# Kernel optimization log

Measured on AMD Instinct MI355X. Metric: run time of the kernel, lower is better.

Reference implementation:

```python
import jax, jax.numpy as jnp
import numpy as np

N_NODES = 50000
N_EDGES = 600000
N_GRAPHS = 1000
IN_DIM, HID, OUT_DIM = 100, 128, 128


def _gcn_layer(x, src, dst, W, b, n_nodes):
    # PyG GCNConv: linear -> symmetric-normalized aggregation with self-loops -> +bias
    h = x @ W                                            # [N, H]
    ones = jnp.ones((src.shape[0],), dtype=h.dtype)
    deg = jax.ops.segment_sum(ones, dst, num_segments=n_nodes) + 1.0  # +1 for self-loop
    dinv = jax.lax.rsqrt(deg)                            # deg >= 1
    norm = dinv[src] * dinv[dst]                         # [E]
    msgs = h[src] * norm[:, None]                        # [E, H] gather + scale
    agg = jax.ops.segment_sum(msgs, dst, num_segments=n_nodes)
    agg = agg + h * (dinv * dinv)[:, None]               # self-loop contribution
    return agg + b


def setup_inputs() -> dict:
    key = jax.random.key(0)
    ks = jax.random.split(key, 9)
    x = jax.random.normal(ks[0], (N_NODES, IN_DIM), dtype=jnp.float32)
    edge_index = jax.random.randint(ks[1], (2, N_EDGES), 0, N_NODES, dtype=jnp.int32)
    batch = jnp.sort(jax.random.randint(ks[2], (N_NODES,), 0, N_GRAPHS, dtype=jnp.int32))
    s = 1.0 / np.sqrt(IN_DIM)
    W1 = jax.random.uniform(ks[3], (IN_DIM, HID), minval=-s, maxval=s, dtype=jnp.float32)
    b1 = jnp.zeros((HID,), dtype=jnp.float32)
    s2 = 1.0 / np.sqrt(HID)
    W2 = jax.random.uniform(ks[4], (HID, HID), minval=-s2, maxval=s2, dtype=jnp.float32)
    b2 = jnp.zeros((HID,), dtype=jnp.float32)
    Wp = jax.random.uniform(ks[5], (HID, OUT_DIM), minval=-s2, maxval=s2, dtype=jnp.float32)
    bp = jax.random.uniform(ks[6], (OUT_DIM,), minval=-s2, maxval=s2, dtype=jnp.float32)
    return {"x": x, "edge_index": edge_index, "batch": batch,
            "W1": W1, "b1": b1, "W2": W2, "b2": b2, "Wp": Wp, "bp": bp}


def reference(x, edge_index, batch, W1, b1, W2, b2, Wp, bp):
    src, dst = edge_index[0], edge_index[1]
    h = jax.nn.relu(_gcn_layer(x, src, dst, W1, b1, N_NODES))   # dropout inactive (eval)
    h = jax.nn.relu(_gcn_layer(h, src, dst, W2, b2, N_NODES))
    # global mean pool over batch segments
    sums = jax.ops.segment_sum(h, batch, num_segments=N_GRAPHS)            # [B, H]
    cnts = jax.ops.segment_sum(jnp.ones_like(batch, dtype=h.dtype), batch,
                               num_segments=N_GRAPHS)
    pooled = sums / jnp.maximum(cnts, 1.0)[:, None]
    return pooled @ Wp + bp                                                # [B, OUT]
```

## Files before the change

kernel.cpp:

```cpp
#include <hip/hip_runtime.h>
#include <hip/hip_bf16.h>

#define N_NODES 50000
#define N_EDGES 600000
#define N_GRAPHS 1000
#define IN_DIM 100
#define HID 128
#define OUT_DIM 128
#define KP 128
#define NDSTRIDE 50048
#define NRANGE 13
#define RSHIFT 12

typedef __attribute__((ext_vector_type(8))) short bf16x8;
typedef __attribute__((ext_vector_type(4))) float f32x4;

__device__ inline unsigned short f2bf(float f) {
    __hip_bfloat16 b = __float2bfloat16(f);
    return *reinterpret_cast<unsigned short*>(&b);
}
__device__ inline float bf2f(unsigned short u) { return __uint_as_float(((unsigned int)u) << 16); }
__device__ inline float bflo(unsigned int u) { return __uint_as_float(u << 16); }
__device__ inline float bfhi(unsigned int u) { return __uint_as_float(u & 0xffff0000u); }

__global__ __launch_bounds__(256) void prep(
    const int* __restrict__ batch,
    const float* __restrict__ W1, const float* __restrict__ W2,
    unsigned short* __restrict__ wt1, unsigned short* __restrict__ wt2,
    int* __restrict__ deg_r, int* __restrict__ total, int* __restrict__ starts,
    float* __restrict__ sums)
{
    const int tid = blockIdx.x * 256 + threadIdx.x;
    const int nth = gridDim.x * 256;

    int4* z = reinterpret_cast<int4*>(deg_r);
    const int nz = (NRANGE * NDSTRIDE) / 4;
    for (int i = tid; i < nz; i += nth) z[i] = make_int4(0, 0, 0, 0);
    int4* zs = reinterpret_cast<int4*>(sums);
    for (int i = tid; i < (N_GRAPHS * HID) / 4; i += nth) zs[i] = make_int4(0, 0, 0, 0);
    if (tid == 0) total[0] = 0;

    for (int idx = tid; idx < 2 * 128 * KP; idx += nth) {
        const float* W = W1; int K = IN_DIM;
        unsigned short* wt = wt1;
        int li = idx;
        if (idx >= 128 * KP) { W = W2; K = HID; wt = wt2; li = idx - 128 * KP; }
        int n = li >> 7;
        int k = li & (KP - 1);
        float v = (k < K) ? W[(size_t)k * 128 + n] : 0.0f;
        unsigned short hi = f2bf(v);
        unsigned short lo = f2bf(v - bf2f(hi));
        size_t o = ((size_t)n << 8) + (size_t)((k >> 3) << 4) + (k & 7);
        wt[o] = hi;
        wt[o + 8] = lo;
    }

    for (int i = tid; i < N_NODES; i += nth) {
        int b = batch[i];
        if (i == 0) {
            for (int g = 0; g <= b; ++g) starts[g] = 0;
        } else {
            int pb = batch[i - 1];
            for (int g = pb + 1; g <= b; ++g) starts[g] = i;
        }
        if (i == N_NODES - 1) {
            for (int g = b + 1; g <= N_GRAPHS; ++g) starts[g] = N_NODES;
        }
    }
}

__global__ __launch_bounds__(256) void deg_count_r(
    const int* __restrict__ src, const int* __restrict__ dst, int* __restrict__ deg_r)
{
    int e = blockIdx.x * 256 + threadIdx.x;
    if (e >= N_EDGES) return;
    int d = dst[e];
    int r = src[e] >> RSHIFT;
    atomicAdd(&deg_r[r * NDSTRIDE + d], 1);
}

__global__ __launch_bounds__(256) void alloc_off_r(
    const int* __restrict__ deg_r, int* __restrict__ off, int* __restrict__ deg,
    int* __restrict__ total, float* __restrict__ dinv, int* __restrict__ cursor_r)
{
    int i = blockIdx.x * 256 + threadIdx.x;
    int pre[NRANGE];
    int v = 0;
    if (i < N_NODES) {
#pragma unroll
        for (int r = 0; r < NRANGE; r++) { pre[r] = v; v += deg_r[r * NDSTRIDE + i]; }
    }
    int lane = threadIdx.x & 63;
    int wid  = threadIdx.x >> 6;
    int x = v;
#pragma unroll
    for (int d = 1; d < 64; d <<= 1) {
        int y = __shfl_up(x, d, 64);
        if (lane >= d) x += y;
    }
    __shared__ int wsum[4];
    __shared__ int wbase[4];
    if (lane == 63) wsum[wid] = x;
    __syncthreads();
    if (threadIdx.x == 0) {
        int s0 = wsum[0], s1 = wsum[1], s2 = wsum[2], s3 = wsum[3];
        int base = atomicAdd(total, s0 + s1 + s2 + s3);
        wbase[0] = base;
        wbase[1] = base + s0;
        wbase[2] = base + s0 + s1;
        wbase[3] = base + s0 + s1 + s2;
    }
    __syncthreads();
    if (i < N_NODES) {
        int base = wbase[wid] + x - v;
        off[i] = base;
        deg[i] = v;
        dinv[i] = rsqrtf((float)v + 1.0f);
#pragma unroll
        for (int r = 0; r < NRANGE; r++) cursor_r[r * NDSTRIDE + i] = base + pre[r];
    }
}

__global__ __launch_bounds__(256) void fill_csr_r(
    const int* __restrict__ src, const int* __restrict__ dst,
    int* __restrict__ cursor_r, int* __restrict__ csr)
{
    int e = blockIdx.x * 256 + threadIdx.x;
    if (e >= N_EDGES) return;
    int d = dst[e];
    int s = src[e];
    int r = s >> RSHIFT;
    int pos = atomicAdd(&cursor_r[r * NDSTRIDE + d], 1);
    csr[pos] = s;
}

__global__ __launch_bounds__(256) void gemm_mfma(
    const float* __restrict__ A, int K, int M,
    const unsigned short* __restrict__ wt,
    const float* __restrict__ dinv, unsigned int* __restrict__ hb)
{
    const int w    = threadIdx.x >> 6;
    const int lane = threadIdx.x & 63;
    const int row_in = lane & 15;
    const int kgrp   = lane >> 4;
    const int wrow = w & 1;
    const int wcol = w >> 1;
    const int m = blockIdx.x * 32 + wrow * 16 + row_in;

    f32x4 acc[4];
#pragma unroll
    for (int j = 0; j < 4; j++) acc[j] = (f32x4){0.f, 0.f, 0.f, 0.f};

    for (int k0 = 0; k0 < K; k0 += 32) {
        int kb = k0 + kgrp * 8;
        float av[8];
#pragma unroll
        for (int i = 0; i < 8; i++) av[i] = 0.f;
        if (m < M) {
            if (kb + 8 <= K) {
                const float4* p = reinterpret_cast<const float4*>(A + (size_t)m * K + kb);
                float4 x0 = p[0], x1 = p[1];
                av[0] = x0.x; av[1] = x0.y; av[2] = x0.z; av[3] = x0.w;
                av[4] = x1.x; av[5] = x1.y; av[6] = x1.z; av[7] = x1.w;
            } else {
#pragma unroll
                for (int i = 0; i < 8; i++)
                    if (kb + i < K) av[i] = A[(size_t)m * K + kb + i];
            }
        }
        union { unsigned short u[8]; bf16x8 v; } ah, al;
#pragma unroll
        for (int i = 0; i < 8; i++) {
            unsigned short h = f2bf(av[i]);
            ah.u[i] = h;
            al.u[i] = f2bf(av[i] - bf2f(h));
        }
        bf16x8 bh[4], bl[4];
#pragma unroll
        for (int j = 0; j < 4; j++) {
            const int nb = wcol * 4 + j;
            const size_t wo = ((size_t)(nb * 16 + row_in) << 8) + (size_t)((kb >> 3) << 4);
            bh[j] = *reinterpret_cast<const bf16x8*>(wt + wo);
            bl[j] = *reinterpret_cast<const bf16x8*>(wt + wo + 8);
        }
#pragma unroll
        for (int j = 0; j < 4; j++) {
            acc[j] = __builtin_amdgcn_mfma_f32_16x16x32_bf16(ah.v, bh[j], acc[j], 0, 0, 0);
            acc[j] = __builtin_amdgcn_mfma_f32_16x16x32_bf16(ah.v, bl[j], acc[j], 0, 0, 0);
            acc[j] = __builtin_amdgcn_mfma_f32_16x16x32_bf16(al.v, bh[j], acc[j], 0, 0, 0);
        }
    }

    __shared__ float C[32][132];
#pragma unroll
    for (int j = 0; j < 4; j++) {
        const int nb = wcol * 4 + j;
#pragma unroll
        for (int r = 0; r < 4; r++)
            C[wrow * 16 + kgrp * 4 + r][nb * 16 + row_in] = acc[j][r];
    }
    __syncthreads();

    int row = threadIdx.x >> 3;
    int c0  = (threadIdx.x & 7) * 16;
    int gm  = blockIdx.x * 32 + row;
    if (gm < M) {
        float dv = dinv[gm];
        unsigned int* orow = hb + (size_t)gm * 64 + (c0 >> 1);
#pragma unroll
        for (int q = 0; q < 2; q++) {
            float4 v0 = *reinterpret_cast<float4*>(&C[row][c0 + q * 8]);
            float4 v1 = *reinterpret_cast<float4*>(&C[row][c0 + q * 8 + 4]);
            uint4 pk;
            pk.x = (unsigned int)f2bf(v0.x * dv) | ((unsigned int)f2bf(v0.y * dv) << 16);
            pk.y = (unsigned int)f2bf(v0.z * dv) | ((unsigned int)f2bf(v0.w * dv) << 16);
            pk.z = (unsigned int)f2bf(v1.x * dv) | ((unsigned int)f2bf(v1.y * dv) << 16);
            pk.w = (unsigned int)f2bf(v1.z * dv) | ((unsigned int)f2bf(v1.w * dv) << 16);
            *reinterpret_cast<uint4*>(orow + q * 4) = pk;
        }
    }
}

__device__ inline void upadd(float* a, uint4 v) {
    a[0] += bflo(v.x); a[1] += bfhi(v.x); a[2] += bflo(v.y); a[3] += bfhi(v.y);
    a[4] += bflo(v.z); a[5] += bfhi(v.z); a[6] += bflo(v.w); a[7] += bfhi(v.w);
}

__device__ inline void gather_rows(
    const uint4* __restrict__ hp, const int* __restrict__ csr,
    int node, int beg, int end, int lane, float* __restrict__ a )
{
    float a0[8], a1[8];
    uint4 self = hp[(size_t)node * 16 + lane];
    a0[0] = bflo(self.x); a0[1] = bfhi(self.x); a0[2] = bflo(self.y); a0[3] = bfhi(self.y);
    a0[4] = bflo(self.z); a0[5] = bfhi(self.z); a0[6] = bflo(self.w); a0[7] = bfhi(self.w);
#pragma unroll
    for (int i = 0; i < 8; i++) a1[i] = 0.f;

    int j = beg;
    for (; j + 7 < end; j += 8) {
        int s0 = csr[j + 0], s1 = csr[j + 1], s2 = csr[j + 2], s3 = csr[j + 3];
        int s4 = csr[j + 4], s5 = csr[j + 5], s6 = csr[j + 6], s7 = csr[j + 7];
        uint4 v0 = hp[(size_t)s0 * 16 + lane];
        uint4 v1 = hp[(size_t)s1 * 16 + lane];
        uint4 v2 = hp[(size_t)s2 * 16 + lane];
        uint4 v3 = hp[(size_t)s3 * 16 + lane];
        uint4 v4 = hp[(size_t)s4 * 16 + lane];
        uint4 v5 = hp[(size_t)s5 * 16 + lane];
        uint4 v6 = hp[(size_t)s6 * 16 + lane];
        uint4 v7 = hp[(size_t)s7 * 16 + lane];
        upadd(a0, v0); upadd(a1, v1); upadd(a0, v2); upadd(a1, v3);
        upadd(a0, v4); upadd(a1, v5); upadd(a0, v6); upadd(a1, v7);
    }
    if (j + 3 < end) {
        int s0 = csr[j + 0], s1 = csr[j + 1], s2 = csr[j + 2], s3 = csr[j + 3];
        uint4 v0 = hp[(size_t)s0 * 16 + lane];
        uint4 v1 = hp[(size_t)s1 * 16 + lane];
        uint4 v2 = hp[(size_t)s2 * 16 + lane];
        uint4 v3 = hp[(size_t)s3 * 16 + lane];
        upadd(a0, v0); upadd(a1, v1); upadd(a0, v2); upadd(a1, v3);
        j += 4;
    }
    for (; j < end; ++j) {
        uint4 v = hp[(size_t)csr[j] * 16 + lane];
        upadd(a0, v);
    }
#pragma unroll
    for (int i = 0; i < 8; i++) a[i] = a0[i] + a1[i];
}

__global__ __launch_bounds__(256) void gather_gemm(
    const uint4* __restrict__ hp, const float* __restrict__ dinv,
    const int* __restrict__ off, const int* __restrict__ deg,
    const int* __restrict__ csr, const float* __restrict__ bias,
    const unsigned short* __restrict__ wt,
    unsigned int* __restrict__ hb_out)
{
    __shared__ float xs[16][132];

    {
        int nl   = threadIdx.x >> 4;
        int lane = threadIdx.x & 15;
        int node = blockIdx.x * 16 + nl;
        int beg = off[node];
        int end = beg + deg[node];
        float dd = dinv[node];

        float a[8];
        gather_rows(hp, csr, node, beg, end, lane, a);

        float r0[4], r1[4];
#pragma unroll
        for (int i = 0; i < 4; i++) {
            r0[i] = fmaxf(fmaf(a[i], dd, bias[lane * 8 + i]), 0.f);
            r1[i] = fmaxf(fmaf(a[4 + i], dd, bias[lane * 8 + 4 + i]), 0.f);
        }
        *reinterpret_cast<float4*>(&xs[nl][lane * 8])     = *reinterpret_cast<float4*>(r0);
        *reinterpret_cast<float4*>(&xs[nl][lane * 8 + 4]) = *reinterpret_cast<float4*>(r1);
    }
    __syncthreads();

    const int w      = threadIdx.x >> 6;
    const int lane   = threadIdx.x & 63;
    const int row_in = lane & 15;
    const int kgrp   = lane >> 4;

    f32x4 acc[2];
    acc[0] = (f32x4){0.f, 0.f, 0.f, 0.f};
    acc[1] = (f32x4){0.f, 0.f, 0.f, 0.f};

#pragma unroll
    for (int k0 = 0; k0 < 128; k0 += 32) {
        int kb = k0 + kgrp * 8;
        float av[8];
        *reinterpret_cast<float4*>(&av[0]) = *reinterpret_cast<const float4*>(&xs[row_in][kb]);
        *reinterpret_cast<float4*>(&av[4]) = *reinterpret_cast<const float4*>(&xs[row_in][kb + 4]);
        union { unsigned short u[8]; bf16x8 v; } ah, al;
#pragma unroll
        for (int i = 0; i < 8; i++) {
            unsigned short h = f2bf(av[i]);
            ah.u[i] = h;
            al.u[i] = f2bf(av[i] - bf2f(h));
        }
#pragma unroll
        for (int j = 0; j < 2; j++) {
            const int nb = w * 2 + j;
            const size_t wo = ((size_t)(nb * 16 + row_in) << 8) + (size_t)((kb >> 3) << 4);
            bf16x8 bh = *reinterpret_cast<const bf16x8*>(wt + wo);
            bf16x8 bl = *reinterpret_cast<const bf16x8*>(wt + wo + 8);
            acc[j] = __builtin_amdgcn_mfma_f32_16x16x32_bf16(ah.v, bh, acc[j], 0, 0, 0);
            acc[j] = __builtin_amdgcn_mfma_f32_16x16x32_bf16(ah.v, bl, acc[j], 0, 0, 0);
            acc[j] = __builtin_amdgcn_mfma_f32_16x16x32_bf16(al.v, bh, acc[j], 0, 0, 0);
        }
    }
    __syncthreads();

#pragma unroll
    for (int j = 0; j < 2; j++) {
        const int nb = w * 2 + j;
#pragma unroll
        for (int r = 0; r < 4; r++)
            xs[kgrp * 4 + r][nb * 16 + row_in] = acc[j][r];
    }
    __syncthreads();

    {
        int row = threadIdx.x >> 4;
        int c0  = (threadIdx.x & 15) * 8;
        int gm  = blockIdx.x * 16 + row;
        float dv = dinv[gm];
        float4 v0 = *reinterpret_cast<float4*>(&xs[row][c0]);
        float4 v1 = *reinterpret_cast<float4*>(&xs[row][c0 + 4]);
        uint4 pk;
        pk.x = (unsigned int)f2bf(v0.x * dv) | ((unsigned int)f2bf(v0.y * dv) << 16);
        pk.y = (unsigned int)f2bf(v0.z * dv) | ((unsigned int)f2bf(v0.w * dv) << 16);
        pk.z = (unsigned int)f2bf(v1.x * dv) | ((unsigned int)f2bf(v1.y * dv) << 16);
        pk.w = (unsigned int)f2bf(v1.z * dv) | ((unsigned int)f2bf(v1.w * dv) << 16);
        *reinterpret_cast<uint4*>(hb_out + (size_t)gm * 64 + (c0 >> 1)) = pk;
    }
}

__global__ __launch_bounds__(256) void gather_pool(
    const uint4* __restrict__ hp, const float* __restrict__ dinv,
    const int* __restrict__ off, const int* __restrict__ deg,
    const int* __restrict__ csr, const float* __restrict__ bias,
    const int* __restrict__ batch, float* __restrict__ sums)
{
    __shared__ float red[16][132];
    __shared__ int gids[16];

    {
        int nl   = threadIdx.x >> 4;
        int lane = threadIdx.x & 15;
        int node = blockIdx.x * 16 + nl;
        int beg = off[node];
        int end = beg + deg[node];
        float dd = dinv[node];

        float a[8];
        gather_rows(hp, csr, node, beg, end, lane, a);

        float r0[4], r1[4];
#pragma unroll
        for (int i = 0; i < 4; i++) {
            r0[i] = fmaxf(fmaf(a[i], dd, bias[lane * 8 + i]), 0.f);
            r1[i] = fmaxf(fmaf(a[4 + i], dd, bias[lane * 8 + 4 + i]), 0.f);
        }
        *reinterpret_cast<float4*>(&red[nl][lane * 8])     = *reinterpret_cast<float4*>(r0);
        *reinterpret_cast<float4*>(&red[nl][lane * 8 + 4]) = *reinterpret_cast<float4*>(r1);
        if (lane == 0) gids[nl] = batch[node];
    }
    __syncthreads();

    if (threadIdx.x < 128) {
        int c = threadIdx.x;
        float acc = red[0][c];
        int curg = gids[0];
        for (int rrow = 1; rrow < 16; ++rrow) {
            int g = gids[rrow];
            if (g == curg) {
                acc += red[rrow][c];
            } else {
                atomicAdd(&sums[(size_t)curg * HID + c], acc);
                curg = g;
                acc = red[rrow][c];
            }
        }
        atomicAdd(&sums[(size_t)curg * HID + c], acc);
    }
}

__global__ __launch_bounds__(128) void head(
    const float* __restrict__ sums, const int* __restrict__ starts,
    const float* __restrict__ Wp, const float* __restrict__ bp,
    float* __restrict__ out)
{
    __shared__ float p[128];
    int g = blockIdx.x;
    int t = threadIdx.x;
    float cnt = (float)(starts[g + 1] - starts[g]);
    p[t] = sums[(size_t)g * HID + t] / fmaxf(cnt, 1.0f);
    __syncthreads();
    float o = bp[t];
#pragma unroll 8
    for (int k = 0; k < HID; k++) o += p[k] * Wp[(size_t)k * OUT_DIM + t];
    out[(size_t)g * OUT_DIM + t] = o;
}

extern "C" void kernel_launch(void* const* d_in, const int* in_sizes, int n_in,
                              void* d_out, int out_size, void* d_ws, size_t ws_size,
                              hipStream_t stream) {
    const float* x   = (const float*)d_in[0];
    const int*   ei  = (const int*)d_in[1];
    const int*   srcp = ei;
    const int*   dstp = ei + N_EDGES;
    const int*   batch = (const int*)d_in[2];
    const float* W1 = (const float*)d_in[3];
    const float* b1 = (const float*)d_in[4];
    const float* W2 = (const float*)d_in[5];
    const float* b2 = (const float*)d_in[6];
    const float* Wp = (const float*)d_in[7];
    const float* bp = (const float*)d_in[8];
    float* out = (float*)d_out;

    float* ws      = (float*)d_ws;
    float* dinv    = ws;
    int*   deg     = (int*)(ws + 50048);
    int*   off     = deg + 50048;
    int*   starts  = off + 50048;
    int*   total   = starts + 1024;
    unsigned short* wt1 = (unsigned short*)(total + 32);
    unsigned short* wt2 = wt1 + 2 * 128 * KP;
    float* sums    = (float*)(wt2 + 2 * 128 * KP);
    int*   deg_r   = (int*)(sums + 128000);
    int*   cursor_r= deg_r + NRANGE * NDSTRIDE;
    int*   csr     = cursor_r + NRANGE * NDSTRIDE;
    unsigned int* hb2 = (unsigned int*)(csr + 600000);
    unsigned int* hb1 = hb2 + 3200000;

    prep<<<512, 256, 0, stream>>>(batch, W1, W2, wt1, wt2, deg_r, total, starts, sums);
    deg_count_r<<<(N_EDGES + 255) / 256, 256, 0, stream>>>(srcp, dstp, deg_r);
    alloc_off_r<<<(N_NODES + 255) / 256, 256, 0, stream>>>(deg_r, off, deg, total, dinv, cursor_r);
    fill_csr_r<<<(N_EDGES + 255) / 256, 256, 0, stream>>>(srcp, dstp, cursor_r, csr);

    gemm_mfma<<<(N_NODES + 31) / 32, 256, 0, stream>>>(x, IN_DIM, N_NODES, wt1, dinv, hb1);

    gather_gemm<<<N_NODES / 16, 256, 0, stream>>>((const uint4*)hb1, dinv, off, deg, csr,
                                                  b1, wt2, hb2);

    gather_pool<<<N_NODES / 16, 256, 0, stream>>>((const uint4*)hb2, dinv, off, deg, csr,
                                                  b2, batch, sums);

    head<<<N_GRAPHS, 128, 0, stream>>>(sums, starts, Wp, bp, out);
}
```

Baseline: 187.5 us.

## Replace range-bucketed CSR build with plain CSR plus per-graph degree-sorted node order

Drops the source-range bucketing (13 range counters per node) that kept each node's neighbour list roughly ordered by source index. The CSR is now built with a single degree array and a single cursor. A new per-graph rank-sort kernel orders nodes by in-degree inside each graph, and both gather kernels process nodes in that order so the 16 nodes in a block have similar neighbour counts. This trades gather locality and one extra kernel launch for better load balance inside each block, plus fewer atomics and less memory traffic during the CSR build.

```diff
diff --git a/kernel.cpp b/kernel.cpp
--- a/kernel.cpp
+++ b/kernel.cpp
@@ -8,9 +8,6 @@
 #define HID 128
 #define OUT_DIM 128
 #define KP 128
-#define NDSTRIDE 50048
-#define NRANGE 13
-#define RSHIFT 12
 
 typedef __attribute__((ext_vector_type(8))) short bf16x8;
 typedef __attribute__((ext_vector_type(4))) float f32x4;
@@ -27,15 +24,14 @@
     const int* __restrict__ batch,
     const float* __restrict__ W1, const float* __restrict__ W2,
     unsigned short* __restrict__ wt1, unsigned short* __restrict__ wt2,
-    int* __restrict__ deg_r, int* __restrict__ total, int* __restrict__ starts,
+    int* __restrict__ deg, int* __restrict__ total, int* __restrict__ starts,
     float* __restrict__ sums)
 {
     const int tid = blockIdx.x * 256 + threadIdx.x;
     const int nth = gridDim.x * 256;
 
-    int4* z = reinterpret_cast<int4*>(deg_r);
-    const int nz = (NRANGE * NDSTRIDE) / 4;
-    for (int i = tid; i < nz; i += nth) z[i] = make_int4(0, 0, 0, 0);
+    int4* z = reinterpret_cast<int4*>(deg);
+    for (int i = tid; i < 50048 / 4; i += nth) z[i] = make_int4(0, 0, 0, 0);
     int4* zs = reinterpret_cast<int4*>(sums);
     for (int i = tid; i < (N_GRAPHS * HID) / 4; i += nth) zs[i] = make_int4(0, 0, 0, 0);
     if (tid == 0) total[0] = 0;
@@ -69,27 +65,36 @@
     }
 }
 
-__global__ __launch_bounds__(256) void deg_count_r(
-    const int* __restrict__ src, const int* __restrict__ dst, int* __restrict__ deg_r)
+__global__ __launch_bounds__(256) void deg_count(
+    const int* __restrict__ dst, int* __restrict__ deg)
 {
     int e = blockIdx.x * 256 + threadIdx.x;
-    if (e >= N_EDGES) return;
-    int d = dst[e];
-    int r = src[e] >> RSHIFT;
-    atomicAdd(&deg_r[r * NDSTRIDE + d], 1);
-}
-
-__global__ __launch_bounds__(256) void alloc_off_r(
-    const int* __restrict__ deg_r, int* __restrict__ off, int* __restrict__ deg,
-    int* __restrict__ total, float* __restrict__ dinv, int* __restrict__ cursor_r)
+    if (e < N_EDGES) atomicAdd(&deg[dst[e]], 1);
+}
+
+__global__ __launch_bounds__(64) void ranksort(
+    const int* __restrict__ starts, const int* __restrict__ deg, int* __restrict__ perm)
+{
+    int g = blockIdx.x;
+    int s0 = starts[g], s1 = starts[g + 1];
+    int n = s1 - s0;
+    for (int i = threadIdx.x; i < n; i += 64) {
+        int di = deg[s0 + i];
+        int r = 0;
+        for (int j = 0; j < n; j++) {
+            int dj = deg[s0 + j];
+            r += (dj < di) || (dj == di && j < i);
+        }
+        perm[s0 + r] = s0 + i;
+    }
+}
+
+__global__ __launch_bounds__(256) void alloc_off(
+    const int* __restrict__ deg, int* __restrict__ off,
+    int* __restrict__ total, float* __restrict__ dinv, int* __restrict__ cursor)
 {
     int i = blockIdx.x * 256 + threadIdx.x;
-    int pre[NRANGE];
-    int v = 0;
-    if (i < N_NODES) {
-#pragma unroll
-        for (int r = 0; r < NRANGE; r++) { pre[r] = v; v += deg_r[r * NDSTRIDE + i]; }
-    }
+    int v = (i < N_NODES) ? deg[i] : 0;
     int lane = threadIdx.x & 63;
     int wid  = threadIdx.x >> 6;
     int x = v;
@@ -114,24 +119,20 @@
     if (i < N_NODES) {
         int base = wbase[wid] + x - v;
         off[i] = base;
-        deg[i] = v;
         dinv[i] = rsqrtf((float)v + 1.0f);
-#pragma unroll
-        for (int r = 0; r < NRANGE; r++) cursor_r[r * NDSTRIDE + i] = base + pre[r];
-    }
-}
-
-__global__ __launch_bounds__(256) void fill_csr_r(
+        cursor[i] = base;
+    }
+}
+
+__global__ __launch_bounds__(256) void fill_csr(
     const int* __restrict__ src, const int* __restrict__ dst,
-    int* __restrict__ cursor_r, int* __restrict__ csr)
+    int* __restrict__ cursor, int* __restrict__ csr)
 {
     int e = blockIdx.x * 256 + threadIdx.x;
     if (e >= N_EDGES) return;
     int d = dst[e];
-    int s = src[e];
-    int r = s >> RSHIFT;
-    int pos = atomicAdd(&cursor_r[r * NDSTRIDE + d], 1);
-    csr[pos] = s;
+    int pos = atomicAdd(&cursor[d], 1);
+    csr[pos] = src[e];
 }
 
 __global__ __launch_bounds__(256) void gemm_mfma(
@@ -272,7 +273,8 @@
 __global__ __launch_bounds__(256) void gather_gemm(
     const uint4* __restrict__ hp, const float* __restrict__ dinv,
     const int* __restrict__ off, const int* __restrict__ deg,
-    const int* __restrict__ csr, const float* __restrict__ bias,
+    const int* __restrict__ csr, const int* __restrict__ perm,
+    const float* __restrict__ bias,
     const unsigned short* __restrict__ wt,
     unsigned int* __restrict__ hb_out)
 {
@@ -281,7 +283,7 @@
     {
         int nl   = threadIdx.x >> 4;
         int lane = threadIdx.x & 15;
-        int node = blockIdx.x * 16 + nl;
+        int node = perm[blockIdx.x * 16 + nl];
         int beg = off[node];
         int end = beg + deg[node];
         float dd = dinv[node];
@@ -347,7 +349,7 @@
     {
         int row = threadIdx.x >> 4;
         int c0  = (threadIdx.x & 15) * 8;
-        int gm  = blockIdx.x * 16 + row;
+        int gm  = perm[blockIdx.x * 16 + row];
         float dv = dinv[gm];
         float4 v0 = *reinterpret_cast<float4*>(&xs[row][c0]);
         float4 v1 = *reinterpret_cast<float4*>(&xs[row][c0 + 4]);
@@ -363,7 +365,8 @@
 __global__ __launch_bounds__(256) void gather_pool(
     const uint4* __restrict__ hp, const float* __restrict__ dinv,
     const int* __restrict__ off, const int* __restrict__ deg,
-    const int* __restrict__ csr, const float* __restrict__ bias,
+    const int* __restrict__ csr, const int* __restrict__ perm,
+    const float* __restrict__ bias,
     const int* __restrict__ batch, float* __restrict__ sums)
 {
     __shared__ float red[16][132];
@@ -372,7 +375,7 @@
     {
         int nl   = threadIdx.x >> 4;
         int lane = threadIdx.x & 15;
-        int node = blockIdx.x * 16 + nl;
+        int node = perm[blockIdx.x * 16 + nl];
         int beg = off[node];
         int end = beg + deg[node];
         float dd = dinv[node];
@@ -447,29 +450,30 @@
     float* dinv    = ws;
     int*   deg     = (int*)(ws + 50048);
     int*   off     = deg + 50048;
-    int*   starts  = off + 50048;
+    int*   perm    = off + 50048;
+    int*   cursor  = perm + 50048;
+    int*   starts  = cursor + 50048;
     int*   total   = starts + 1024;
     unsigned short* wt1 = (unsigned short*)(total + 32);
     unsigned short* wt2 = wt1 + 2 * 128 * KP;
     float* sums    = (float*)(wt2 + 2 * 128 * KP);
-    int*   deg_r   = (int*)(sums + 128000);
-    int*   cursor_r= deg_r + NRANGE * NDSTRIDE;
-    int*   csr     = cursor_r + NRANGE * NDSTRIDE;
+    int*   csr     = (int*)(sums + 128000);
     unsigned int* hb2 = (unsigned int*)(csr + 600000);
     unsigned int* hb1 = hb2 + 3200000;
 
-    prep<<<512, 256, 0, stream>>>(batch, W1, W2, wt1, wt2, deg_r, total, starts, sums);
-    deg_count_r<<<(N_EDGES + 255) / 256, 256, 0, stream>>>(srcp, dstp, deg_r);
-    alloc_off_r<<<(N_NODES + 255) / 256, 256, 0, stream>>>(deg_r, off, deg, total, dinv, cursor_r);
-    fill_csr_r<<<(N_EDGES + 255) / 256, 256, 0, stream>>>(srcp, dstp, cursor_r, csr);
+    prep<<<512, 256, 0, stream>>>(batch, W1, W2, wt1, wt2, deg, total, starts, sums);
+    deg_count<<<(N_EDGES + 255) / 256, 256, 0, stream>>>(dstp, deg);
+    ranksort<<<N_GRAPHS, 64, 0, stream>>>(starts, deg, perm);
+    alloc_off<<<(N_NODES + 255) / 256, 256, 0, stream>>>(deg, off, total, dinv, cursor);
+    fill_csr<<<(N_EDGES + 255) / 256, 256, 0, stream>>>(srcp, dstp, cursor, csr);
 
     gemm_mfma<<<(N_NODES + 31) / 32, 256, 0, stream>>>(x, IN_DIM, N_NODES, wt1, dinv, hb1);
 
     gather_gemm<<<N_NODES / 16, 256, 0, stream>>>((const uint4*)hb1, dinv, off, deg, csr,
-                                                  b1, wt2, hb2);
+                                                  perm, b1, wt2, hb2);
 
     gather_pool<<<N_NODES / 16, 256, 0, stream>>>((const uint4*)hb2, dinv, off, deg, csr,
-                                                  b2, batch, sums);
+                                                  perm, b2, batch, sums);
 
     head<<<N_GRAPHS, 128, 0, stream>>>(sums, starts, Wp, bp, out);
 }
```

Result: slower. 198.4 us (+5.8%).
